# Optimization experiments

Hardware: AMD Instinct MI355X
Metric: run time of the kernel (lower is better)

Reference implementation:

```python
import jax, jax.numpy as jnp
import numpy as np

B, L = 4, 2048
D_MODEL = 64          # d_model = input_size
ED = 128              # d_inner = expand_factor * d_model = hidden_size
N = 32                # d_state
DCONV = 16            # d_conv
NLAYERS = 4
DTRANK = 4            # ceil(d_model/16)
NCLS = 1
EPS = 1e-5


def setup_inputs() -> dict:
    key = jax.random.key(0)
    ks = jax.random.split(key, 10)
    g = lambda k, s, sc: jax.random.normal(k, s, dtype=jnp.float32) * sc
    inp = {}
    inp["x"] = jax.random.normal(ks[0], (B, L, D_MODEL), dtype=jnp.float32)
    inp["in_w"] = g(ks[1], (NLAYERS, 2 * ED, D_MODEL), 0.1)
    inp["in_b"] = jnp.zeros((NLAYERS, 2 * ED), jnp.float32)
    inp["conv_w"] = g(ks[2], (NLAYERS, ED, 1, DCONV), 0.1)  # depthwise kernel (OIH per group)
    inp["conv_b"] = jnp.zeros((NLAYERS, ED), jnp.float32)
    inp["xproj_w"] = g(ks[3], (NLAYERS, DTRANK + 2 * N, ED), 0.1)
    inp["dtproj_w"] = g(ks[4], (NLAYERS, ED, DTRANK), 0.5)
    inp["dtproj_b"] = g(ks[5], (NLAYERS, ED), 0.5)
    # S4D-real init: A[e, n] = n+1
    A = jnp.tile(jnp.arange(1, N + 1, dtype=jnp.float32), (ED, 1))
    inp["A_log"] = jnp.tile(jnp.log(A)[None], (NLAYERS, 1, 1))
    inp["Dp"] = jnp.ones((NLAYERS, ED), jnp.float32)
    inp["outproj_w"] = g(ks[6], (NLAYERS, D_MODEL, ED), 0.1)
    inp["outproj_b"] = jnp.zeros((NLAYERS, D_MODEL), jnp.float32)
    inp["norm_w"] = jnp.ones((NLAYERS, D_MODEL), jnp.float32)
    inp["fc_w"] = g(ks[7], (NCLS, ED), 0.1)
    inp["fc_b"] = jnp.zeros((NCLS,), jnp.float32)
    return inp


def _rmsnorm(x, w):
    return x * jax.lax.rsqrt(jnp.mean(x * x, axis=-1, keepdims=True) + EPS) * w


def _causal_dwconv(x, w, b):
    # x: [B,L,ED], w: [ED,1,DCONV] depthwise, causal left pad
    xt = jnp.swapaxes(x, 1, 2)  # [B,ED,L]
    y = jax.lax.conv_general_dilated(
        xt, w, window_strides=(1,), padding=[(DCONV - 1, 0)],
        dimension_numbers=("NCH", "OIH", "NCH"), feature_group_count=ED)
    return jnp.swapaxes(y, 1, 2) + b


def _mamba_block(h, in_w, in_b, conv_w, conv_b, xproj_w, dtproj_w, dtproj_b,
                 A_log, Dp, outproj_w, outproj_b, last):
    xz = jnp.einsum("bld,ed->ble", h, in_w) + in_b          # [B,L,2ED]
    xin, z = jnp.split(xz, 2, axis=-1)
    xc = jax.nn.silu(_causal_dwconv(xin, conv_w, conv_b))    # [B,L,ED]
    dbc = jnp.einsum("ble,re->blr", xc, xproj_w)             # [B,L,DTRANK+2N]
    delta = dbc[..., :DTRANK]
    Bm = dbc[..., DTRANK:DTRANK + N]                          # [B,L,N]
    Cm = dbc[..., DTRANK + N:]                                # [B,L,N]
    delta = jax.nn.softplus(jnp.einsum("blr,er->ble", delta, dtproj_w) + dtproj_b)
    A = -jnp.exp(A_log)                                       # [ED,N]
    dA = jnp.exp(delta[..., None] * A)                        # [B,L,ED,N]
    dBu = delta[..., None] * Bm[:, :, None, :] * xc[..., None]  # [B,L,ED,N]

    def step(hs, t):
        dA_t, dBu_t, C_t = t                                  # [B,ED,N],[B,ED,N],[B,N]
        hs = dA_t * hs + dBu_t
        y = jnp.einsum("ben,bn->be", hs, C_t)
        return hs, y

    h0 = jnp.zeros((xc.shape[0], ED, N), dtype=xc.dtype)
    _, ys = jax.lax.scan(step, h0, (jnp.swapaxes(dA, 0, 1),
                                    jnp.swapaxes(dBu, 0, 1),
                                    jnp.swapaxes(Cm, 0, 1)))
    y = jnp.swapaxes(ys, 0, 1) + Dp * xc                      # [B,L,ED]
    y = y * jax.nn.silu(z)
    if last:
        return y                                              # classifier taps d_inner features
    return jnp.einsum("ble,de->bld", y, outproj_w) + outproj_b


def reference(x, in_w, in_b, conv_w, conv_b, xproj_w, dtproj_w, dtproj_b,
              A_log, Dp, outproj_w, outproj_b, norm_w, fc_w, fc_b):
    h = x
    for i in range(NLAYERS - 1):
        h = h + _mamba_block(_rmsnorm(h, norm_w[i]), in_w[i], in_b[i], conv_w[i],
                             conv_b[i], xproj_w[i], dtproj_w[i], dtproj_b[i],
                             A_log[i], Dp[i], outproj_w[i], outproj_b[i], False)
    i = NLAYERS - 1
    y = _mamba_block(_rmsnorm(h, norm_w[i]), in_w[i], in_b[i], conv_w[i],
                     conv_b[i], xproj_w[i], dtproj_w[i], dtproj_b[i],
                     A_log[i], Dp[i], outproj_w[i], outproj_b[i], True)
    last_hidden = y[:, -1, :]                                 # [B,ED]
    return last_hidden @ fc_w.T + fc_b                        # [B,NCLS]
```

## Files before the change

### kernel.cpp

```cpp
#include <hip/hip_runtime.h>
#include <math.h>

#define BSZ 4
#define Lseq 2048
#define DM 64
#define ED 128
#define NST 32
#define DCONVK 16
#define NLAYERS 4
#define DTRANK 4
#define EPSV 1e-5f
#define NC 128
#define TT 16
#define NSEG 8
#define GRIDN (BSZ * NC)
#define L2E 1.4426950408889634f

#if defined(__has_builtin)
#if __has_builtin(__builtin_amdgcn_exp2f)
#define EXP2F(x) __builtin_amdgcn_exp2f(x)
#else
#define EXP2F(x) exp2f(x)
#endif
#else
#define EXP2F(x) exp2f(x)
#endif

__device__ __forceinline__ float sigf(float x) { return 1.0f / (1.0f + __expf(-x)); }
__device__ __forceinline__ float hsum4(float4 a) { return (a.x + a.y) + (a.z + a.w); }

__device__ __forceinline__ float ldsc(const float* p) {
    return __hip_atomic_load((float*)p, __ATOMIC_RELAXED, __HIP_MEMORY_SCOPE_AGENT);
}
__device__ __forceinline__ void stsc(float* p, float v) {
    __hip_atomic_store(p, v, __ATOMIC_RELAXED, __HIP_MEMORY_SCOPE_AGENT);
}
__device__ __forceinline__ unsigned long long ldsc64(const void* p) {
    return __hip_atomic_load((unsigned long long*)p, __ATOMIC_RELAXED,
                             __HIP_MEMORY_SCOPE_AGENT);
}
__device__ __forceinline__ void stsc64(void* p, unsigned long long v) {
    __hip_atomic_store((unsigned long long*)p, v, __ATOMIC_RELAXED,
                       __HIP_MEMORY_SCOPE_AGENT);
}

__device__ __forceinline__ void gbar(unsigned int* cnt8, unsigned int* rel,
                                     unsigned int k)
{
    __syncthreads();
    if (blockIdx.x == 0) {
        if (threadIdx.x == 0)
            __hip_atomic_fetch_add(&cnt8[0], 1u, __ATOMIC_RELAXED,
                                   __HIP_MEMORY_SCOPE_AGENT);
        if (threadIdx.x < 8) {
            while (__hip_atomic_load(&cnt8[threadIdx.x * 64], __ATOMIC_RELAXED,
                                     __HIP_MEMORY_SCOPE_AGENT) < k * 64u)
                __builtin_amdgcn_s_sleep(1);
        }
        __syncthreads();
        __hip_atomic_store(&rel[threadIdx.x * 16], k,
                           __ATOMIC_RELAXED, __HIP_MEMORY_SCOPE_AGENT);
        __hip_atomic_store(&rel[(threadIdx.x + 256) * 16], k,
                           __ATOMIC_RELAXED, __HIP_MEMORY_SCOPE_AGENT);
    } else {
        if (threadIdx.x == 0) {
            __hip_atomic_fetch_add(&cnt8[(blockIdx.x & 7) * 64], 1u,
                                   __ATOMIC_RELAXED, __HIP_MEMORY_SCOPE_AGENT);
            while (__hip_atomic_load(&rel[blockIdx.x * 16], __ATOMIC_RELAXED,
                                     __HIP_MEMORY_SCOPE_AGENT) < k)
                __builtin_amdgcn_s_sleep(2);
        }
    }
    __builtin_amdgcn_sched_barrier(0);
    __syncthreads();
}

__device__ __forceinline__ void inproj16(
    const float* in_w_l, const float* in_b_l, const float (*hn)[DM],
    float* xin, float* zbuf, float* haloW, float* zbH_b, bool lastChunk,
    size_t t0, int tid)
{
    float4 w4[16];
    const float4* wr = (const float4*)(in_w_l + tid * DM);
    #pragma unroll
    for (int i = 0; i < 16; ++i) w4[i] = wr[i];
    const float bias = in_b_l[tid];
    #pragma unroll 2
    for (int tok = 0; tok < TT; ++tok) {
        const float4* hv4 = (const float4*)&hn[tok][0];
        float4 a4 = make_float4(0.f, 0.f, 0.f, 0.f);
        #pragma unroll
        for (int i = 0; i < 16; ++i) {
            float4 hv = hv4[i];
            a4.x = fmaf(hv.x, w4[i].x, a4.x);
            a4.y = fmaf(hv.y, w4[i].y, a4.y);
            a4.z = fmaf(hv.z, w4[i].z, a4.z);
            a4.w = fmaf(hv.w, w4[i].w, a4.w);
        }
        const float r = bias + hsum4(a4);
        if (tid < ED) {
            xin[(t0 + tok) * ED + tid] = r;
            if (tok >= 1) stsc(&haloW[(tok - 1) * ED + tid], r);
        } else {
            zbuf[(t0 + tok) * ED + (tid - ED)] = r;
            if (lastChunk && tok == TT - 1) stsc(&zbH_b[tid - ED], r);
        }
    }
}

struct KParams {
    const float *x, *in_w, *in_b, *conv_w, *conv_b, *xproj_w, *dtproj_w,
                *dtproj_b, *A_log, *Dp, *outproj_w, *outproj_b, *norm_w,
                *fc_w, *fc_b;
    float *out, *h0, *h1, *xin, *zbuf, *xc, *dlt, *Bv, *Cv, *dsum, *hloc,
          *H, *zbH;
    unsigned int *cnt, *rel;
};

__global__ __launch_bounds__(256, 2) void k_mamba(KParams P)
{
    const int bid = blockIdx.x;
    const int tid = threadIdx.x;
    unsigned int bk = 0;
    __shared__ __align__(16) float smem[12288];

    if (bid == 0 && tid < BSZ) stsc(&P.out[tid], 0.f);

    const bool lastChunk = (bid & 127) == (NC - 1);
    float* haloW = P.H + (size_t)bid * ((DCONVK - 1) * ED);
    float* zbH_b = P.zbH + (size_t)(bid >> 7) * ED;

    {
        float (*hn)[DM] = (float (*)[DM])smem;
        const size_t t0 = (size_t)bid * TT;
        const int lane = tid & 63, wv = tid >> 6;
        const float nw = P.norm_w[lane];
        float hval[4];
        #pragma unroll
        for (int j = 0; j < 4; ++j)
            hval[j] = P.x[(t0 + wv * 4 + j) * DM + lane];
        #pragma unroll
        for (int j = 0; j < 4; ++j) {
            float ss = hval[j] * hval[j];
            #pragma unroll
            for (int off = 32; off; off >>= 1) ss += __shfl_xor(ss, off, 64);
            const float sc = rsqrtf(ss * (1.0f / DM) + EPSV);
            hn[wv * 4 + j][lane] = hval[j] * sc * nw;
        }
        __syncthreads();
        inproj16(P.in_w, P.in_b, (const float (*)[DM])hn, P.xin, P.zbuf,
                 haloW, zbH_b, lastChunk, t0, tid);
    }
    gbar(P.cnt, P.rel, ++bk);

    #pragma unroll 1
    for (int li = 0; li < NLAYERS; ++li) {
        const int last = (li == NLAYERS - 1);
        const float* Alog = P.A_log + (size_t)li * ED * NST;
        const float* Dpl  = P.Dp + (size_t)li * ED;

        {
            const int b = bid >> 7, c = bid & 127;
            const int l0 = c * TT;
            const size_t t0 = (size_t)b * Lseq + l0;
            const int e = tid & 127, half = tid >> 7;
            const int store_dbc = last ? 0 : 1;
            const bool doXC = store_dbc || (c == NC - 1);

            float* xs = smem;
            float (*xcs)[ED] = (float (*)[ED])(smem + 4096);
            float (*Bs)[NST] = (float (*)[NST])(smem + 6144);
            float (*dts)[DTRANK] = (float (*)[DTRANK])(smem + 6656);
            float* hsT = smem + 6720;
            float (*dl)[ED] = (float (*)[ED])xs;

            const float* conv_w   = P.conv_w + (size_t)li * ED * DCONVK;
            const float* conv_b   = P.conv_b + (size_t)li * ED;
            const float* xproj_w  = P.xproj_w + (size_t)li * (DTRANK + 2 * NST) * ED;
            const float* dtproj_w = P.dtproj_w + (size_t)li * ED * DTRANK;
            const float* dtproj_b = P.dtproj_b + (size_t)li * ED;

            float Aen16[16];
            {
                const float4* a4 = (const float4*)(Alog + e * NST + half * 16);
                #pragma unroll
                for (int i = 0; i < 4; ++i) {
                    float4 v = a4[i];
                    Aen16[i*4+0] = -__expf(v.x) * L2E; Aen16[i*4+1] = -__expf(v.y) * L2E;
                    Aen16[i*4+2] = -__expf(v.z) * L2E; Aen16[i*4+3] = -__expf(v.w) * L2E;
                }
            }
            float w[DCONVK];
            {
                const float4* cw = (const float4*)(conv_w + e * DCONVK);
                #pragma unroll
                for (int i = 0; i < 4; ++i) {
                    float4 cc = cw[i];
                    w[i*4+0] = cc.x; w[i*4+1] = cc.y; w[i*4+2] = cc.z; w[i*4+3] = cc.w;
                }
            }
            const float cb = conv_b[e];

            {
                float hv[8];
                #pragma unroll
                for (int i = 0; i < 8; ++i) {
                    const int idx = tid + i * 256;
                    float val = 0.f;
                    if (idx < (DCONVK - 1) * ED && c > 0)
                        val = ldsc(P.H + (size_t)(bid - 1) * ((DCONVK - 1) * ED) + idx);
                    hv[i] = val;
                }
                float4 ov[2];
                #pragma unroll
                for (int i = 0; i < 2; ++i) {
                    const int idx4 = 480 + tid + i * 256;
                    const int row = idx4 >> 5;
                    const int lrow = l0 - (DCONVK - 1) + row;
                    ov[i] = ((const float4*)(P.xin + ((size_t)b * Lseq + lrow) * ED))[idx4 & 31];
                }
                #pragma unroll
                for (int i = 0; i < 8; ++i) {
                    const int idx = tid + i * 256;
                    if (idx < (DCONVK - 1) * ED) xs[idx] = hv[i];
                }
                #pragma unroll
                for (int i = 0; i < 2; ++i)
                    ((float4*)xs)[480 + tid + i * 256] = ov[i];
            }
            __syncthreads();

            {
                #pragma unroll 2
                for (int j = 0; j < 8; ++j) {
                    const int tok = half * 8 + j;
                    float acc = cb;
                    #pragma unroll
                    for (int k = 0; k < DCONVK; ++k)
                        acc = fmaf(xs[(tok + k) * ED + e], w[k], acc);
                    const float xcv = acc * sigf(acc);
                    xcs[tok][e] = xcv;
                    if (doXC) {
                        if (store_dbc) P.xc[(t0 + tok) * ED + e] = xcv;
                        else           stsc(&P.xc[(t0 + tok) * ED + e], xcv);
                    }
                }
            }
            __syncthreads();

            {
                const int wv = tid >> 6, lane = tid & 63;
                float4 acc[4];
                #pragma unroll
                for (int j = 0; j < 4; ++j) acc[j] = make_float4(0.f, 0.f, 0.f, 0.f);
                #pragma unroll 1
                for (int p = 0; p < 4; ++p) {
                    float4 w4[8];
                    const float4* wr = (const float4*)(xproj_w + lane * ED + p * 32);
                    #pragma unroll
                    for (int i = 0; i < 8; ++i) w4[i] = wr[i];
                    #pragma unroll
                    for (int j = 0; j < 4; ++j) {
                        const float4* yv = (const float4*)&xcs[wv * 4 + j][p * 32];
                        #pragma unroll
                        for (int i = 0; i < 8; ++i) {
                            float4 hv = yv[i];
                            acc[j].x = fmaf(hv.x, w4[i].x, acc[j].x);
                            acc[j].y = fmaf(hv.y, w4[i].y, acc[j].y);
                            acc[j].z = fmaf(hv.z, w4[i].z, acc[j].z);
                            acc[j].w = fmaf(hv.w, w4[i].w, acc[j].w);
                        }
                    }
                }
                #pragma unroll
                for (int j = 0; j < 4; ++j) {
                    const int tok = wv * 4 + j;
                    const float v = hsum4(acc[j]);
                    if (lane < DTRANK) {
                        dts[tok][lane] = v;
                    } else if (lane < DTRANK + NST) {
                        Bs[tok][lane - DTRANK] = v;
                        if (store_dbc) P.Bv[(t0 + tok) * NST + (lane - DTRANK)] = v;
                    } else {
                        if (doXC) {
                            const int ci = lane - DTRANK - NST;
                            if (store_dbc) P.Cv[(t0 + tok) * NST + ci] = v;
                            else           stsc(&P.Cv[(t0 + tok) * NST + ci], v);
                        }
                    }
                }
                {
                    const int ridx = lane & 3;
                    const int ks   = (lane >> 2) & 3;
                    const int tsub = lane >> 4;
                    const int r4   = 64 + ridx;
                    const int tok  = wv * 4 + tsub;
                    const float4* wr = (const float4*)(xproj_w + r4 * ED + ks * 32);
                    const float4* yv = (const float4*)&xcs[tok][ks * 32];
                    float4 a4 = make_float4(0.f, 0.f, 0.f, 0.f);
                    #pragma unroll
                    for (int i = 0; i < 8; ++i) {
                        float4 hv = yv[i]; float4 wv4 = wr[i];
                        a4.x = fmaf(hv.x, wv4.x, a4.x);
                        a4.y = fmaf(hv.y, wv4.y, a4.y);
                        a4.z = fmaf(hv.z, wv4.z, a4.z);
                        a4.w = fmaf(hv.w, wv4.w, a4.w);
                    }
                    float v = hsum4(a4);
                    v += __shfl_xor(v, 4, 64);
                    v += __shfl_xor(v, 8, 64);
                    if (ks == 0 && doXC) {
                        const int ci = r4 - DTRANK - NST;
                        if (store_dbc) P.Cv[(t0 + tok) * NST + ci] = v;
                        else           stsc(&P.Cv[(t0 + tok) * NST + ci], v);
                    }
                }
            }
            __syncthreads();

            {
                const float4 dwv = *(const float4*)(dtproj_w + e * DTRANK);
                const float bias = dtproj_b[e];
                #pragma unroll 2
                for (int j = 0; j < 8; ++j) {
                    const int tok = half * 8 + j;
                    float a = bias;
                    a = fmaf(dts[tok][0], dwv.x, a);
                    a = fmaf(dts[tok][1], dwv.y, a);
                    a = fmaf(dts[tok][2], dwv.z, a);
                    a = fmaf(dts[tok][3], dwv.w, a);
                    const float sp = fmaxf(a, 0.f) + log1pf(__expf(-fabsf(a)));
                    dl[tok][e] = sp;
                    if (store_dbc) P.dlt[(t0 + tok) * ED + e] = sp;
                }
            }
            __syncthreads();

            {
                float dsum = 0.f;
                #pragma unroll 4
                for (int l = 0; l < TT; ++l) dsum += dl[l][e];
                if (half == 0) stsc(&P.dsum[((size_t)b * NC + c) * ED + e], dsum);

                #pragma unroll 1
                for (int g = 0; g < 2; ++g) {
                    const int n0 = half * 16 + g * 8;
                    float Aen[8];
                    #pragma unroll
                    for (int k = 0; k < 8; ++k) Aen[k] = Aen16[g * 8 + k];
                    float hs[8];
                    #pragma unroll
                    for (int k = 0; k < 8; ++k) hs[k] = 0.f;
                    #pragma unroll 2
                    for (int l = 0; l < TT; ++l) {
                        const float de   = dl[l][e];
                        const float dexc = de * xcs[l][e];
                        const float4 B0 = *(const float4*)&Bs[l][n0];
                        const float4 B1 = *(const float4*)&Bs[l][n0 + 4];
                        float a;
                        a = EXP2F(de * Aen[0]); hs[0] = fmaf(a, hs[0], B0.x * dexc);
                        a = EXP2F(de * Aen[1]); hs[1] = fmaf(a, hs[1], B0.y * dexc);
                        a = EXP2F(de * Aen[2]); hs[2] = fmaf(a, hs[2], B0.z * dexc);
                        a = EXP2F(de * Aen[3]); hs[3] = fmaf(a, hs[3], B0.w * dexc);
                        a = EXP2F(de * Aen[4]); hs[4] = fmaf(a, hs[4], B1.x * dexc);
                        a = EXP2F(de * Aen[5]); hs[5] = fmaf(a, hs[5], B1.y * dexc);
                        a = EXP2F(de * Aen[6]); hs[6] = fmaf(a, hs[6], B1.z * dexc);
                        a = EXP2F(de * Aen[7]); hs[7] = fmaf(a, hs[7], B1.w * dexc);
                    }
                    #pragma unroll
                    for (int k = 0; k < 8; ++k) hsT[e * 33 + n0 + k] = hs[k];
                }
                __syncthreads();
                {
                    unsigned long long* dst =
                        (unsigned long long*)(P.hloc + (size_t)bid * (ED * NST));
                    #pragma unroll
                    for (int it = 0; it < 8; ++it) {
                        const int idx = tid + it * 256;
                        const int ee = idx >> 4;
                        const int nn = (idx & 15) * 2;
                        union { float f[2]; unsigned long long u; } pk;
                        pk.f[0] = hsT[ee * 33 + nn];
                        pk.f[1] = hsT[ee * 33 + nn + 1];
                        stsc64(dst + idx, pk.u);
                    }
                }
            }
        }
        gbar(P.cnt, P.rel, ++bk);

        {
            const int tt  = tid & 31;
            const int seg = tid >> 5;
            const int t   = bid * 32 + tt;
            const int b   = t >> 12;
            const int en  = t & 4095;
            const int e   = en >> 5;

            const float Aen2 = -__expf(Alog[en]) * L2E;

            const int c0 = seg * (NC / NSEG);
            const size_t idxBase = (size_t)b * NC * (ED * NST) + en;
            const size_t dBase   = (size_t)b * NC * ED + e;

            float u[NC / NSEG], a[NC / NSEG];
            #pragma unroll
            for (int k = 0; k < NC / NSEG; ++k)
                u[k] = ldsc(P.hloc + idxBase + (size_t)(c0 + k) * (ED * NST));
            #pragma unroll
            for (int k = 0; k < NC / NSEG; ++k)
                a[k] = EXP2F(Aen2 * ldsc(P.dsum + dBase + (size_t)(c0 + k) * ED));

            float A = 1.f, U = 0.f;
            #pragma unroll
            for (int k = 0; k < NC / NSEG; ++k) { U = fmaf(a[k], U, u[k]); A *= a[k]; }

            float (*As)[32] = (float (*)[32])smem;
            float (*Us)[32] = (float (*)[32])(smem + NSEG * 32);
            As[seg][tt] = A; Us[seg][tt] = U;
            __syncthreads();

            float h = 0.f;
            #pragma unroll
            for (int j = 0; j < NSEG - 1; ++j)
                if (j < seg) h = fmaf(As[j][tt], h, Us[j][tt]);

            #pragma unroll
            for (int k = 0; k < NC / NSEG; ++k) {
                stsc(P.hloc + idxBase + (size_t)(c0 + k) * (ED * NST), h);
                h = fmaf(a[k], h, u[k]);
            }

            if (last && seg == NSEG - 1) {
                const int n = en & 31;
                const size_t tok = (size_t)b * Lseq + (Lseq - 1);
                float p = h * ldsc(P.Cv + tok * NST + n);
                #pragma unroll
                for (int off = 16; off; off >>= 1) p += __shfl_xor(p, off, 32);
                if (n == 0) {
                    const float xce = ldsc(P.xc + tok * ED + e);
                    const float zi  = ldsc(P.zbH + (size_t)b * ED + e);
                    float val = (p + Dpl[e] * xce) * (zi * sigf(zi)) * P.fc_w[e];
                    if (en == 0) val += P.fc_b[0];
                    atomicAdd(&P.out[b], val);
                }
            }
        }

        if (!last) {
            gbar(P.cnt, P.rel, ++bk);
            {
                const int b = bid >> 7, c = bid & 127;
                const int l0 = c * TT;
                const size_t t0 = (size_t)b * Lseq + l0;
                const int e = tid & 127, half = tid >> 7;

                float (*dlS)[ED] = (float (*)[ED])(smem);
                float (*xcS)[ED] = (float (*)[ED])(smem + 2048);
                float (*BsS)[NST] = (float (*)[NST])(smem + 4096);
                float (*CsS)[NST] = (float (*)[NST])(smem + 4608);
                float (*ys)[ED]  = (float (*)[ED])(smem + 5120);
                float (*pp)[TT][ED] = (float (*)[TT][ED])(smem + 7168);
                float (*hn)[DM]  = (float (*)[DM])(smem + 11264);

                const float* ow = P.outproj_w + (size_t)li * DM * ED;
                const float* ob = P.outproj_b + (size_t)li * DM;
                const float* hres = (li == 0) ? P.x : ((li == 1) ? P.h0 : P.h1);
                float* hout = (li & 1) ? P.h1 : P.h0;

                float Aen16[16];
                {
                    const float4* a4 = (const float4*)(Alog + e * NST + half * 16);
                    #pragma unroll
                    for (int i = 0; i < 4; ++i) {
                        float4 v = a4[i];
                        Aen16[i*4+0] = -__expf(v.x) * L2E; Aen16[i*4+1] = -__expf(v.y) * L2E;
                        Aen16[i*4+2] = -__expf(v.z) * L2E; Aen16[i*4+3] = -__expf(v.w) * L2E;
                    }
                }

                float hs16[16];
                {
                    const size_t idx = (size_t)bid * (ED * NST) + e * NST + half * 16;
                    const unsigned long long* src =
                        (const unsigned long long*)(P.hloc + idx);
                    #pragma unroll
                    for (int k = 0; k < 8; ++k) {
                        union { float f[2]; unsigned long long u; } pk;
                        pk.u = ldsc64(src + k);
                        hs16[2 * k]     = pk.f[0];
                        hs16[2 * k + 1] = pk.f[1];
                    }
                }

                {
                    const float4* dsrc = (const float4*)(P.dlt + t0 * ED);
                    const float4* xsrc = (const float4*)(P.xc + t0 * ED);
                    float4* ddst = (float4*)&dlS[0][0];
                    float4* xdst = (float4*)&xcS[0][0];
                    #pragma unroll
                    for (int i = 0; i < 2; ++i) {
                        ddst[tid + i * 256] = dsrc[tid + i * 256];
                        xdst[tid + i * 256] = xsrc[tid + i * 256];
                    }
                    if (tid < 128) {
                        ((float4*)&BsS[0][0])[tid] = ((const float4*)(P.Bv + t0 * NST))[tid];
                        ((float4*)&CsS[0][0])[tid] = ((const float4*)(P.Cv + t0 * NST))[tid];
                    }
                }
                __syncthreads();

                #pragma unroll 1
                for (int g = 0; g < 2; ++g) {
                    const int n0 = half * 16 + g * 8;
                    float Aen[8];
                    #pragma unroll
                    for (int k = 0; k < 8; ++k) Aen[k] = Aen16[g * 8 + k];
                    float hs[8];
                    #pragma unroll
                    for (int k = 0; k < 8; ++k) hs[k] = hs16[g * 8 + k];
                    #pragma unroll 2
                    for (int l = 0; l < TT; ++l) {
                        const float de   = dlS[l][e];
                        const float dexc = de * xcS[l][e];
                        const float4 B0 = *(const float4*)&BsS[l][n0];
                        const float4 B1 = *(const float4*)&BsS[l][n0 + 4];
                        const float4 C0 = *(const float4*)&CsS[l][n0];
                        const float4 C1 = *(const float4*)&CsS[l][n0 + 4];
                        float a, p = 0.f;
                        a = EXP2F(de * Aen[0]); hs[0] = fmaf(a, hs[0], B0.x * dexc); p = fmaf(hs[0], C0.x, p);
                        a = EXP2F(de * Aen[1]); hs[1] = fmaf(a, hs[1], B0.y * dexc); p = fmaf(hs[1], C0.y, p);
                        a = EXP2F(de * Aen[2]); hs[2] = fmaf(a, hs[2], B0.z * dexc); p = fmaf(hs[2], C0.z, p);
                        a = EXP2F(de * Aen[3]); hs[3] = fmaf(a, hs[3], B0.w * dexc); p = fmaf(hs[3], C0.w, p);
                        a = EXP2F(de * Aen[4]); hs[4] = fmaf(a, hs[4], B1.x * dexc); p = fmaf(hs[4], C1.x, p);
                        a = EXP2F(de * Aen[5]); hs[5] = fmaf(a, hs[5], B1.y * dexc); p = fmaf(hs[5], C1.y, p);
                        a = EXP2F(de * Aen[6]); hs[6] = fmaf(a, hs[6], B1.z * dexc); p = fmaf(hs[6], C1.z, p);
                        a = EXP2F(de * Aen[7]); hs[7] = fmaf(a, hs[7], B1.w * dexc); p = fmaf(hs[7], C1.w, p);
                        if (g == 0) pp[half][l][e] = p;
                        else        pp[half][l][e] += p;
                    }
                }
                __syncthreads();
                {
                    const float dpe = Dpl[e];
                    #pragma unroll 2
                    for (int j = 0; j < 8; ++j) {
                        const int tl = half * 8 + j;
                        const size_t tok = t0 + tl;
                        const float p = pp[0][tl][e] + pp[1][tl][e];
                        const float zi = P.zbuf[tok * ED + e];
                        ys[tl][e] = (p + dpe * xcS[tl][e]) * (zi * sigf(zi));
                    }
                }
                __syncthreads();

                const int lane = tid & 63;
                const int wv = tid >> 6;
                const float nw = P.norm_w[(size_t)(li + 1) * DM + lane];
                float hval[4];
                {
                    float4 acc[4];
                    #pragma unroll
                    for (int j = 0; j < 4; ++j) acc[j] = make_float4(0.f, 0.f, 0.f, 0.f);
                    #pragma unroll 1
                    for (int p = 0; p < 4; ++p) {
                        float4 w4[8];
                        const float4* wr = (const float4*)(ow + lane * ED + p * 32);
                        #pragma unroll
                        for (int q = 0; q < 8; ++q) w4[q] = wr[q];
                        #pragma unroll
                        for (int j = 0; j < 4; ++j) {
                            const float4* yv = (const float4*)&ys[wv * 4 + j][p * 32];
                            #pragma unroll
                            for (int q = 0; q < 8; ++q) {
                                float4 hv = yv[q];
                                acc[j].x = fmaf(hv.x, w4[q].x, acc[j].x);
                                acc[j].y = fmaf(hv.y, w4[q].y, acc[j].y);
                                acc[j].z = fmaf(hv.z, w4[q].z, acc[j].z);
                                acc[j].w = fmaf(hv.w, w4[q].w, acc[j].w);
                            }
                        }
                    }
                    const float obd = ob[lane];
                    #pragma unroll
                    for (int j = 0; j < 4; ++j) {
                        const size_t tok = t0 + wv * 4 + j;
                        hval[j] = hsum4(acc[j]) + obd + hres[tok * DM + lane];
                        hout[tok * DM + lane] = hval[j];
                    }
                }
                #pragma unroll
                for (int j = 0; j < 4; ++j) {
                    float ss = hval[j] * hval[j];
                    #pragma unroll
                    for (int off = 32; off; off >>= 1) ss += __shfl_xor(ss, off, 64);
                    const float sc = rsqrtf(ss * (1.0f / DM) + EPSV);
                    hn[wv * 4 + j][lane] = hval[j] * sc * nw;
                }
                __syncthreads();
                inproj16(P.in_w + (size_t)(li + 1) * 2 * ED * DM,
                         P.in_b + (size_t)(li + 1) * 2 * ED,
                         (const float (*)[DM])hn, P.xin, P.zbuf,
                         haloW, zbH_b, lastChunk, t0, tid);
            }
            gbar(P.cnt, P.rel, ++bk);
        }
    }
}

extern "C" void kernel_launch(void* const* d_in, const int* in_sizes, int n_in,
                              void* d_out, int out_size, void* d_ws, size_t ws_size,
                              hipStream_t stream)
{
    const size_t TOK = (size_t)BSZ * Lseq;
    float* ws = (float*)d_ws;
    float* h0    = ws; ws += TOK * DM;
    float* h1    = ws; ws += TOK * DM;
    float* xin   = ws; ws += TOK * ED;
    float* zbuf  = ws; ws += TOK * ED;
    float* xc    = ws; ws += TOK * ED;
    float* dlt   = ws; ws += TOK * ED;
    float* Bv    = ws; ws += TOK * NST;
    float* Cv    = ws; ws += TOK * NST;
    float* dsum  = ws; ws += (size_t)BSZ * NC * ED;
    float* hloc  = ws; ws += (size_t)BSZ * NC * ED * NST;
    float* H     = ws; ws += (size_t)GRIDN * (DCONVK - 1) * ED;
    float* zbH   = ws; ws += (size_t)BSZ * ED;
    unsigned int* cnt = (unsigned int*)ws;
    unsigned int* rel = cnt + 8 * 64;

    KParams prm;
    prm.x         = (const float*)d_in[0];
    prm.in_w      = (const float*)d_in[1];
    prm.in_b      = (const float*)d_in[2];
    prm.conv_w    = (const float*)d_in[3];
    prm.conv_b    = (const float*)d_in[4];
    prm.xproj_w   = (const float*)d_in[5];
    prm.dtproj_w  = (const float*)d_in[6];
    prm.dtproj_b  = (const float*)d_in[7];
    prm.A_log     = (const float*)d_in[8];
    prm.Dp        = (const float*)d_in[9];
    prm.outproj_w = (const float*)d_in[10];
    prm.outproj_b = (const float*)d_in[11];
    prm.norm_w    = (const float*)d_in[12];
    prm.fc_w      = (const float*)d_in[13];
    prm.fc_b      = (const float*)d_in[14];
    prm.out  = (float*)d_out;
    prm.h0 = h0; prm.h1 = h1; prm.xin = xin; prm.zbuf = zbuf;
    prm.xc = xc; prm.dlt = dlt; prm.Bv = Bv; prm.Cv = Cv;
    prm.dsum = dsum; prm.hloc = hloc; prm.H = H; prm.zbH = zbH;
    prm.cnt = cnt; prm.rel = rel;

    hipMemsetAsync(cnt, 0, (8 * 64 + 512 * 16) * sizeof(unsigned int), stream);
    k_mamba<<<dim3(GRIDN), dim3(256), 0, stream>>>(prm);
}
```

Baseline: 370.6 us.

## Replace grid-wide barriers with per-batch counters and neighbor halo flags

The single grid-wide barrier is replaced by per-batch counter barriers, so each batch's 128 blocks synchronize only among themselves. The barrier after the in-projection is replaced by a point-to-point flag: each block waits only for its left neighbor's conv halo, and the local xin rows are prefetched before that wait. The output zeroing moves to a host memset. This removes global synchronization latency and lets batches and chunks drift apart, at the cost of relying on relaxed atomics to order memory correctly between blocks.

Measured after the change: 396.2 us. 6.9% more time.

```diff
diff --git a/kernel.cpp b/kernel.cpp
--- a/kernel.cpp
+++ b/kernel.cpp
@@ -43,33 +43,18 @@
     __hip_atomic_store((unsigned long long*)p, v, __ATOMIC_RELAXED,
                        __HIP_MEMORY_SCOPE_AGENT);
 }
-
-__device__ __forceinline__ void gbar(unsigned int* cnt8, unsigned int* rel,
-                                     unsigned int k)
+__device__ __forceinline__ unsigned int ldu(const unsigned int* p) {
+    return __hip_atomic_load((unsigned int*)p, __ATOMIC_RELAXED,
+                             __HIP_MEMORY_SCOPE_AGENT);
+}
+
+__device__ __forceinline__ void bbar(unsigned int* cnt, unsigned int target)
 {
     __syncthreads();
-    if (blockIdx.x == 0) {
-        if (threadIdx.x == 0)
-            __hip_atomic_fetch_add(&cnt8[0], 1u, __ATOMIC_RELAXED,
-                                   __HIP_MEMORY_SCOPE_AGENT);
-        if (threadIdx.x < 8) {
-            while (__hip_atomic_load(&cnt8[threadIdx.x * 64], __ATOMIC_RELAXED,
-                                     __HIP_MEMORY_SCOPE_AGENT) < k * 64u)
-                __builtin_amdgcn_s_sleep(1);
-        }
-        __syncthreads();
-        __hip_atomic_store(&rel[threadIdx.x * 16], k,
-                           __ATOMIC_RELAXED, __HIP_MEMORY_SCOPE_AGENT);
-        __hip_atomic_store(&rel[(threadIdx.x + 256) * 16], k,
-                           __ATOMIC_RELAXED, __HIP_MEMORY_SCOPE_AGENT);
-    } else {
-        if (threadIdx.x == 0) {
-            __hip_atomic_fetch_add(&cnt8[(blockIdx.x & 7) * 64], 1u,
-                                   __ATOMIC_RELAXED, __HIP_MEMORY_SCOPE_AGENT);
-            while (__hip_atomic_load(&rel[blockIdx.x * 16], __ATOMIC_RELAXED,
-                                     __HIP_MEMORY_SCOPE_AGENT) < k)
-                __builtin_amdgcn_s_sleep(2);
-        }
+    if (threadIdx.x == 0) {
+        __hip_atomic_fetch_add(cnt, 1u, __ATOMIC_RELAXED, __HIP_MEMORY_SCOPE_AGENT);
+        while (ldu(cnt) < target)
+            __builtin_amdgcn_s_sleep(1);
     }
     __builtin_amdgcn_sched_barrier(0);
     __syncthreads();
@@ -114,21 +99,21 @@
                 *fc_w, *fc_b;
     float *out, *h0, *h1, *xin, *zbuf, *xc, *dlt, *Bv, *Cv, *dsum, *hloc,
           *H, *zbH;
-    unsigned int *cnt, *rel;
+    unsigned int *cntA, *cntB, *hflag;
 };
 
 __global__ __launch_bounds__(256, 2) void k_mamba(KParams P)
 {
     const int bid = blockIdx.x;
     const int tid = threadIdx.x;
-    unsigned int bk = 0;
+    const int bb = bid >> 7, cc = bid & 127;
     __shared__ __align__(16) float smem[12288];
 
-    if (bid == 0 && tid < BSZ) stsc(&P.out[tid], 0.f);
-
-    const bool lastChunk = (bid & 127) == (NC - 1);
+    const bool lastChunk = (cc == NC - 1);
     float* haloW = P.H + (size_t)bid * ((DCONVK - 1) * ED);
-    float* zbH_b = P.zbH + (size_t)(bid >> 7) * ED;
+    float* zbH_b = P.zbH + (size_t)bb * ED;
+    unsigned int* cA = P.cntA + bb * 64;
+    unsigned int* cB = P.cntB + bb * 64;
 
     {
         float (*hn)[DM] = (float (*)[DM])smem;
@@ -151,7 +136,10 @@
         inproj16(P.in_w, P.in_b, (const float (*)[DM])hn, P.xin, P.zbuf,
                  haloW, zbH_b, lastChunk, t0, tid);
     }
-    gbar(P.cnt, P.rel, ++bk);
+    __syncthreads();
+    if (tid == 0)
+        __hip_atomic_store(&P.hflag[bid * 16], 1u, __ATOMIC_RELAXED,
+                           __HIP_MEMORY_SCOPE_AGENT);
 
     #pragma unroll 1
     for (int li = 0; li < NLAYERS; ++li) {
@@ -160,7 +148,7 @@
         const float* Dpl  = P.Dp + (size_t)li * ED;
 
         {
-            const int b = bid >> 7, c = bid & 127;
+            const int b = bb, c = cc;
             const int l0 = c * TT;
             const size_t t0 = (size_t)b * Lseq + l0;
             const int e = tid & 127, half = tid >> 7;
@@ -195,12 +183,31 @@
                 const float4* cw = (const float4*)(conv_w + e * DCONVK);
                 #pragma unroll
                 for (int i = 0; i < 4; ++i) {
-                    float4 cc = cw[i];
-                    w[i*4+0] = cc.x; w[i*4+1] = cc.y; w[i*4+2] = cc.z; w[i*4+3] = cc.w;
+                    float4 cc4 = cw[i];
+                    w[i*4+0] = cc4.x; w[i*4+1] = cc4.y; w[i*4+2] = cc4.z; w[i*4+3] = cc4.w;
                 }
             }
             const float cb = conv_b[e];
 
+            {
+                float4 ov[2];
+                #pragma unroll
+                for (int i = 0; i < 2; ++i) {
+                    const int idx4 = 480 + tid + i * 256;
+                    const int row = idx4 >> 5;
+                    const int lrow = l0 - (DCONVK - 1) + row;
+                    ov[i] = ((const float4*)(P.xin + ((size_t)b * Lseq + lrow) * ED))[idx4 & 31];
+                }
+                #pragma unroll
+                for (int i = 0; i < 2; ++i)
+                    ((float4*)xs)[480 + tid + i * 256] = ov[i];
+            }
+            if (tid == 0 && c > 0) {
+                while (ldu(&P.hflag[(bid - 1) * 16]) < (unsigned)(li + 1))
+                    __builtin_amdgcn_s_sleep(2);
+            }
+            __builtin_amdgcn_sched_barrier(0);
+            __syncthreads();
             {
                 float hv[8];
                 #pragma unroll
@@ -211,22 +218,11 @@
                         val = ldsc(P.H + (size_t)(bid - 1) * ((DCONVK - 1) * ED) + idx);
                     hv[i] = val;
                 }
-                float4 ov[2];
-                #pragma unroll
-                for (int i = 0; i < 2; ++i) {
-                    const int idx4 = 480 + tid + i * 256;
-                    const int row = idx4 >> 5;
-                    const int lrow = l0 - (DCONVK - 1) + row;
-                    ov[i] = ((const float4*)(P.xin + ((size_t)b * Lseq + lrow) * ED))[idx4 & 31];
-                }
                 #pragma unroll
                 for (int i = 0; i < 8; ++i) {
                     const int idx = tid + i * 256;
                     if (idx < (DCONVK - 1) * ED) xs[idx] = hv[i];
                 }
-                #pragma unroll
-                for (int i = 0; i < 2; ++i)
-                    ((float4*)xs)[480 + tid + i * 256] = ov[i];
             }
             __syncthreads();
 
@@ -387,7 +383,7 @@
                 }
             }
         }
-        gbar(P.cnt, P.rel, ++bk);
+        bbar(cA, (unsigned)(li + 1) * 128u);
 
         {
             const int tt  = tid & 31;
@@ -448,9 +444,9 @@
         }
 
         if (!last) {
-            gbar(P.cnt, P.rel, ++bk);
-            {
-                const int b = bid >> 7, c = bid & 127;
+            bbar(cB, (unsigned)(li + 1) * 128u);
+            {
+                const int b = bb, c = cc;
                 const int l0 = c * TT;
                 const size_t t0 = (size_t)b * Lseq + l0;
                 const int e = tid & 127, half = tid >> 7;
@@ -603,7 +599,10 @@
                          (const float (*)[DM])hn, P.xin, P.zbuf,
                          haloW, zbH_b, lastChunk, t0, tid);
             }
-            gbar(P.cnt, P.rel, ++bk);
+            __syncthreads();
+            if (tid == 0)
+                __hip_atomic_store(&P.hflag[bid * 16], (unsigned)(li + 2),
+                                   __ATOMIC_RELAXED, __HIP_MEMORY_SCOPE_AGENT);
         }
     }
 }
@@ -626,8 +625,9 @@
     float* hloc  = ws; ws += (size_t)BSZ * NC * ED * NST;
     float* H     = ws; ws += (size_t)GRIDN * (DCONVK - 1) * ED;
     float* zbH   = ws; ws += (size_t)BSZ * ED;
-    unsigned int* cnt = (unsigned int*)ws;
-    unsigned int* rel = cnt + 8 * 64;
+    unsigned int* cntA  = (unsigned int*)ws;
+    unsigned int* cntB  = cntA + BSZ * 64;
+    unsigned int* hflag = cntB + BSZ * 64;
 
     KParams prm;
     prm.x         = (const float*)d_in[0];
@@ -649,8 +649,10 @@
     prm.h0 = h0; prm.h1 = h1; prm.xin = xin; prm.zbuf = zbuf;
     prm.xc = xc; prm.dlt = dlt; prm.Bv = Bv; prm.Cv = Cv;
     prm.dsum = dsum; prm.hloc = hloc; prm.H = H; prm.zbH = zbH;
-    prm.cnt = cnt; prm.rel = rel;
-
-    hipMemsetAsync(cnt, 0, (8 * 64 + 512 * 16) * sizeof(unsigned int), stream);
+    prm.cntA = cntA; prm.cntB = cntB; prm.hflag = hflag;
+
+    hipMemsetAsync(d_out, 0, (size_t)BSZ * sizeof(float), stream);
+    hipMemsetAsync(cntA, 0, (size_t)(2 * BSZ * 64 + 512 * 16) * sizeof(unsigned int),
+                   stream);
     k_mamba<<<dim3(GRIDN), dim3(256), 0, stream>>>(prm);
 }
```
